# Performance work log

Measured on AMD Instinct MI355X. Metric: run time of the kernel, lower is better.

## Reference

```python
import jax, jax.numpy as jnp
import numpy as np

NBITS = 8  # num_bits_m1 == num_bits_m2 == 8


def _ste_round(x):
    # straight-through estimator round (gradient = identity)
    return x + jax.lax.stop_gradient(jnp.round(x) - x)


def _pact_quantize(x, clip_val, clip_valn, nbits):
    """PACT-style asymmetric quant-dequant with zero alignment (align_zero=True).

    clamp to [clip_valn, clip_val], affine-quantize to [0, 2^n - 1] with a
    rounded zero point, then dequantize.
    """
    levels = jnp.asarray(2 ** nbits - 1, dtype=x.dtype)
    scale = levels / (clip_val - clip_valn)
    zero_point = _ste_round(-clip_valn * scale)  # align zero to an integer level
    xc = jnp.clip(x, clip_valn, clip_val)
    q = _ste_round(xc * scale + zero_point)
    return (q - zero_point) / scale


def setup_inputs() -> dict:
    key = jax.random.key(0)
    k1, k2 = jax.random.split(key)
    B, H, S, D = 2, 16, 1024, 128
    m1 = jax.random.normal(k1, (B, H, S, D), dtype=jnp.float32)
    m2 = jax.random.normal(k2, (B, H, D, S), dtype=jnp.float32)
    return {
        "m1": m1,
        "m2": m2,
        "m1_clip_val": jnp.asarray(1.0, dtype=jnp.float32),
        "m1_clip_valn": jnp.asarray(-1.0, dtype=jnp.float32),
        "m2_clip_val": jnp.asarray(1.0, dtype=jnp.float32),
        "m2_clip_valn": jnp.asarray(-1.0, dtype=jnp.float32),
    }


def reference(m1, m2, m1_clip_val, m1_clip_valn, m2_clip_val, m2_clip_valn):
    qm1 = _pact_quantize(m1, m1_clip_val, m1_clip_valn, NBITS)
    qm2 = _pact_quantize(m2, m2_clip_val, m2_clip_valn, NBITS)
    # replaceBmm=True path: torch.matmul on [B,H,S,D] x [B,H,D,S]
    return jnp.einsum("bhsd,bhdt->bhst", qm1, qm2)
```

## Files before the change

kernel.cpp:

```cpp
#include <hip/hip_runtime.h>

typedef __attribute__((ext_vector_type(8))) short short8;
typedef __attribute__((ext_vector_type(4))) float floatx4;

__device__ __forceinline__ unsigned short quant_bf16(float x, float cvn, float cv,
                                                     float scale, float zp) {
    float xc = fminf(fmaxf(x, cvn), cv);
    float q  = rintf(xc * scale + zp);
    float v  = q - zp;
    return (unsigned short)(__float_as_uint(v) >> 16);
}

__global__ __launch_bounds__(256) void quant_m1_kernel(
        const float* __restrict__ x, unsigned short* __restrict__ q,
        const float* __restrict__ cvp, const float* __restrict__ cvnp, int n4) {
    int i = blockIdx.x * 256 + threadIdx.x;
    if (i >= n4) return;
    float cv = cvp[0], cvn = cvnp[0];
    float scale = 255.0f / (cv - cvn);
    float zp = rintf(-cvn * scale);
    floatx4 v = ((const floatx4*)x)[i];
    ushort4 o;
    o.x = quant_bf16(v[0], cvn, cv, scale, zp);
    o.y = quant_bf16(v[1], cvn, cv, scale, zp);
    o.z = quant_bf16(v[2], cvn, cv, scale, zp);
    o.w = quant_bf16(v[3], cvn, cv, scale, zp);
    ((ushort4*)q)[i] = o;
}

__global__ __launch_bounds__(256) void quant_m2t_kernel(
        const float* __restrict__ x, unsigned short* __restrict__ qt,
        const float* __restrict__ cvp, const float* __restrict__ cvnp) {
    __shared__ unsigned short ldsT[64][136];
    int batch = blockIdx.y;
    int s0 = blockIdx.x * 64;
    const float* xb = x + (size_t)batch * (128 * 1024);
    unsigned short* qb = qt + (size_t)batch * (1024 * 128);
    float cv = cvp[0], cvn = cvnp[0];
    float scale = 255.0f / (cv - cvn);
    float zp = rintf(-cvn * scale);
    int t = threadIdx.x;
#pragma unroll
    for (int r = 0; r < 2; ++r) {
        int u = t + 256 * r;
        int su = u & 15;
        int du = u >> 4;
        floatx4 v[4];
#pragma unroll
        for (int i = 0; i < 4; ++i)
            v[i] = *(const floatx4*)(xb + (size_t)(du * 4 + i) * 1024 + s0 + su * 4);
#pragma unroll
        for (int j = 0; j < 4; ++j) {
            ushort4 w;
            w.x = quant_bf16(v[0][j], cvn, cv, scale, zp);
            w.y = quant_bf16(v[1][j], cvn, cv, scale, zp);
            w.z = quant_bf16(v[2][j], cvn, cv, scale, zp);
            w.w = quant_bf16(v[3][j], cvn, cv, scale, zp);
            *(ushort4*)&ldsT[su * 4 + j][du * 4] = w;
        }
    }
    __syncthreads();
#pragma unroll
    for (int r = 0; r < 4; ++r) {
        int c = t + 256 * r;
        int sl = c >> 4, k8 = c & 15;
        *(short8*)(qb + (size_t)(s0 + sl) * 128 + k8 * 8) =
            *(const short8*)&ldsT[sl][k8 * 8];
    }
}

__global__ __launch_bounds__(256) void qbmm_kernel(
        const unsigned short* __restrict__ qA, const unsigned short* __restrict__ qBt,
        float* __restrict__ C,
        const float* __restrict__ cv1p, const float* __restrict__ cvn1p,
        const float* __restrict__ cv2p, const float* __restrict__ cvn2p) {
    int batch = blockIdx.z;
    const unsigned short* A  = qA  + (size_t)batch * (1024 * 128);
    const unsigned short* Bt = qBt + (size_t)batch * (1024 * 128);
    float* Cb = C + (size_t)batch * (1024 * 1024);
    int m0 = blockIdx.y * 128, n0 = blockIdx.x * 128;
    int tid = threadIdx.x;
    int lane = tid & 63, w = tid >> 6;
    int wr = w >> 1, wc = w & 1;
    int row16 = lane & 15, quad = lane >> 4;
    int wm = m0 + wr * 64, wn = n0 + wc * 64;

    floatx4 acc[4][4] = {};

    const short8* Ap[4];
    const short8* Bp[4];
#pragma unroll
    for (int i = 0; i < 4; ++i) {
        Ap[i] = (const short8*)(A  + (size_t)(wm + i * 16 + row16) * 128 + quad * 8);
        Bp[i] = (const short8*)(Bt + (size_t)(wn + i * 16 + row16) * 128 + quad * 8);
    }

#pragma unroll
    for (int kk = 0; kk < 4; ++kk) {
        short8 a[4], b[4];
#pragma unroll
        for (int i = 0; i < 4; ++i) { a[i] = Ap[i][kk * 4]; b[i] = Bp[i][kk * 4]; }
#pragma unroll
        for (int mi = 0; mi < 4; ++mi)
#pragma unroll
            for (int ni = 0; ni < 4; ++ni)
                acc[mi][ni] = __builtin_amdgcn_mfma_f32_16x16x32_bf16(
                    b[ni], a[mi], acc[mi][ni], 0, 0, 0);
    }

    float inv = (cv1p[0] - cvn1p[0]) * (cv2p[0] - cvn2p[0]) * (1.0f / 65025.0f);

#pragma unroll
    for (int mi = 0; mi < 4; ++mi) {
        int s = wm + mi * 16 + row16;
        float* crow = Cb + (size_t)s * 1024;
#pragma unroll
        for (int ni = 0; ni < 4; ++ni) {
            floatx4 o = acc[mi][ni] * inv;
            *(floatx4*)(crow + wn + ni * 16 + quad * 4) = o;
        }
    }
}

extern "C" void kernel_launch(void* const* d_in, const int* in_sizes, int n_in,
                              void* d_out, int out_size, void* d_ws, size_t ws_size,
                              hipStream_t stream) {
    const float* m1   = (const float*)d_in[0];
    const float* m2   = (const float*)d_in[1];
    const float* cv1  = (const float*)d_in[2];
    const float* cvn1 = (const float*)d_in[3];
    const float* cv2  = (const float*)d_in[4];
    const float* cvn2 = (const float*)d_in[5];
    float* out = (float*)d_out;

    unsigned short* qA  = (unsigned short*)d_ws;
    unsigned short* qBt = qA + 4194304;

    quant_m1_kernel<<<4096, 256, 0, stream>>>(m1, qA, cv1, cvn1, 1048576);
    quant_m2t_kernel<<<dim3(16, 32), 256, 0, stream>>>(m2, qBt, cv2, cvn2);
    qbmm_kernel<<<dim3(8, 8, 32), 256, 0, stream>>>(qA, qBt, out,
                                                    cv1, cvn1, cv2, cvn2);
}
```

Measured before the change: 191.9 us.

## Fuse quantization of both operands into the batched matmul kernel via LDS

Replaces the two quantization kernels and the separate GEMM with one kernel that loads fp32 tiles of m1 and m2, quantizes them to bf16, stages them (m2 transposed) in shared memory, then runs the MFMA loop from LDS. This removes the workspace write/read round trip and two kernel launches. In exchange each input tile is re-read and re-quantized by every block that uses it, and the larger LDS footprint may reduce occupancy.

```diff
diff --git a/kernel.cpp b/kernel.cpp
--- a/kernel.cpp
+++ b/kernel.cpp
@@ -2,6 +2,8 @@
 
 typedef __attribute__((ext_vector_type(8))) short short8;
 typedef __attribute__((ext_vector_type(4))) float floatx4;
+
+#define LDS_STRIDE 136
 
 __device__ __forceinline__ unsigned short quant_bf16(float x, float cvn, float cv,
                                                      float scale, float zp) {
@@ -11,95 +13,81 @@
     return (unsigned short)(__float_as_uint(v) >> 16);
 }
 
-__global__ __launch_bounds__(256) void quant_m1_kernel(
-        const float* __restrict__ x, unsigned short* __restrict__ q,
-        const float* __restrict__ cvp, const float* __restrict__ cvnp, int n4) {
-    int i = blockIdx.x * 256 + threadIdx.x;
-    if (i >= n4) return;
-    float cv = cvp[0], cvn = cvnp[0];
-    float scale = 255.0f / (cv - cvn);
-    float zp = rintf(-cvn * scale);
-    floatx4 v = ((const floatx4*)x)[i];
-    ushort4 o;
-    o.x = quant_bf16(v[0], cvn, cv, scale, zp);
-    o.y = quant_bf16(v[1], cvn, cv, scale, zp);
-    o.z = quant_bf16(v[2], cvn, cv, scale, zp);
-    o.w = quant_bf16(v[3], cvn, cv, scale, zp);
-    ((ushort4*)q)[i] = o;
-}
+__global__ __launch_bounds__(256) void fused_qbmm_kernel(
+        const float* __restrict__ m1, const float* __restrict__ m2,
+        float* __restrict__ C,
+        const float* __restrict__ cv1p, const float* __restrict__ cvn1p,
+        const float* __restrict__ cv2p, const float* __restrict__ cvn2p) {
+    __shared__ __align__(16) unsigned short As[128 * LDS_STRIDE];
+    __shared__ __align__(16) unsigned short Bs[128 * LDS_STRIDE];
 
-__global__ __launch_bounds__(256) void quant_m2t_kernel(
-        const float* __restrict__ x, unsigned short* __restrict__ qt,
-        const float* __restrict__ cvp, const float* __restrict__ cvnp) {
-    __shared__ unsigned short ldsT[64][136];
-    int batch = blockIdx.y;
-    int s0 = blockIdx.x * 64;
-    const float* xb = x + (size_t)batch * (128 * 1024);
-    unsigned short* qb = qt + (size_t)batch * (1024 * 128);
-    float cv = cvp[0], cvn = cvnp[0];
-    float scale = 255.0f / (cv - cvn);
-    float zp = rintf(-cvn * scale);
-    int t = threadIdx.x;
+    const int batch = blockIdx.z;
+    const int m0 = blockIdx.y * 128, n0 = blockIdx.x * 128;
+    const float* Am = m1 + (size_t)batch * (1024 * 128) + (size_t)m0 * 128;
+    const float* Bm = m2 + (size_t)batch * (128 * 1024) + n0;
+    float* Cb = C + (size_t)batch * (1024 * 1024);
+
+    const float cv1 = cv1p[0], cvn1 = cvn1p[0];
+    const float cv2 = cv2p[0], cvn2 = cvn2p[0];
+    const float s1 = 255.0f / (cv1 - cvn1);
+    const float zp1 = rintf(-cvn1 * s1);
+    const float s2 = 255.0f / (cv2 - cvn2);
+    const float zp2 = rintf(-cvn2 * s2);
+
+    const int tid = threadIdx.x;
+
+    {
+        const int col4 = tid & 31, r0 = tid >> 5;
 #pragma unroll
-    for (int r = 0; r < 2; ++r) {
-        int u = t + 256 * r;
-        int su = u & 15;
-        int du = u >> 4;
-        floatx4 v[4];
+        for (int r = 0; r < 16; ++r) {
+            const int s = r * 8 + r0;
+            floatx4 v = *(const floatx4*)(Am + (size_t)s * 128 + col4 * 4);
+            ushort4 o;
+            o.x = quant_bf16(v[0], cvn1, cv1, s1, zp1);
+            o.y = quant_bf16(v[1], cvn1, cv1, s1, zp1);
+            o.z = quant_bf16(v[2], cvn1, cv1, s1, zp1);
+            o.w = quant_bf16(v[3], cvn1, cv1, s1, zp1);
+            *(ushort4*)&As[s * LDS_STRIDE + col4 * 4] = o;
+        }
+    }
+    {
+        const int t4 = tid & 31, d0 = tid >> 5;
 #pragma unroll
-        for (int i = 0; i < 4; ++i)
-            v[i] = *(const floatx4*)(xb + (size_t)(du * 4 + i) * 1024 + s0 + su * 4);
+        for (int r = 0; r < 4; ++r) {
+            const int d4 = r * 8 + d0;
+            floatx4 v[4];
 #pragma unroll
-        for (int j = 0; j < 4; ++j) {
-            ushort4 w;
-            w.x = quant_bf16(v[0][j], cvn, cv, scale, zp);
-            w.y = quant_bf16(v[1][j], cvn, cv, scale, zp);
-            w.z = quant_bf16(v[2][j], cvn, cv, scale, zp);
-            w.w = quant_bf16(v[3][j], cvn, cv, scale, zp);
-            *(ushort4*)&ldsT[su * 4 + j][du * 4] = w;
+            for (int i = 0; i < 4; ++i)
+                v[i] = *(const floatx4*)(Bm + (size_t)(d4 * 4 + i) * 1024 + t4 * 4);
+#pragma unroll
+            for (int j = 0; j < 4; ++j) {
+                ushort4 w;
+                w.x = quant_bf16(v[0][j], cvn2, cv2, s2, zp2);
+                w.y = quant_bf16(v[1][j], cvn2, cv2, s2, zp2);
+                w.z = quant_bf16(v[2][j], cvn2, cv2, s2, zp2);
+                w.w = quant_bf16(v[3][j], cvn2, cv2, s2, zp2);
+                *(ushort4*)&Bs[(t4 * 4 + j) * LDS_STRIDE + d4 * 4] = w;
+            }
         }
     }
     __syncthreads();
-#pragma unroll
-    for (int r = 0; r < 4; ++r) {
-        int c = t + 256 * r;
-        int sl = c >> 4, k8 = c & 15;
-        *(short8*)(qb + (size_t)(s0 + sl) * 128 + k8 * 8) =
-            *(const short8*)&ldsT[sl][k8 * 8];
-    }
-}
 
-__global__ __launch_bounds__(256) void qbmm_kernel(
-        const unsigned short* __restrict__ qA, const unsigned short* __restrict__ qBt,
-        float* __restrict__ C,
-        const float* __restrict__ cv1p, const float* __restrict__ cvn1p,
-        const float* __restrict__ cv2p, const float* __restrict__ cvn2p) {
-    int batch = blockIdx.z;
-    const unsigned short* A  = qA  + (size_t)batch * (1024 * 128);
-    const unsigned short* Bt = qBt + (size_t)batch * (1024 * 128);
-    float* Cb = C + (size_t)batch * (1024 * 1024);
-    int m0 = blockIdx.y * 128, n0 = blockIdx.x * 128;
-    int tid = threadIdx.x;
-    int lane = tid & 63, w = tid >> 6;
-    int wr = w >> 1, wc = w & 1;
-    int row16 = lane & 15, quad = lane >> 4;
-    int wm = m0 + wr * 64, wn = n0 + wc * 64;
+    const int lane = tid & 63, w = tid >> 6;
+    const int wr = w >> 1, wc = w & 1;
+    const int row16 = lane & 15, quad = lane >> 4;
 
     floatx4 acc[4][4] = {};
-
-    const short8* Ap[4];
-    const short8* Bp[4];
-#pragma unroll
-    for (int i = 0; i < 4; ++i) {
-        Ap[i] = (const short8*)(A  + (size_t)(wm + i * 16 + row16) * 128 + quad * 8);
-        Bp[i] = (const short8*)(Bt + (size_t)(wn + i * 16 + row16) * 128 + quad * 8);
-    }
+    const unsigned short* Abase = &As[(wr * 64 + row16) * LDS_STRIDE + quad * 8];
+    const unsigned short* Bbase = &Bs[(wc * 64 + row16) * LDS_STRIDE + quad * 8];
 
 #pragma unroll
     for (int kk = 0; kk < 4; ++kk) {
         short8 a[4], b[4];
 #pragma unroll
-        for (int i = 0; i < 4; ++i) { a[i] = Ap[i][kk * 4]; b[i] = Bp[i][kk * 4]; }
+        for (int i = 0; i < 4; ++i) {
+            a[i] = *(const short8*)(Abase + i * 16 * LDS_STRIDE + kk * 32);
+            b[i] = *(const short8*)(Bbase + i * 16 * LDS_STRIDE + kk * 32);
+        }
 #pragma unroll
         for (int mi = 0; mi < 4; ++mi)
 #pragma unroll
@@ -108,16 +96,15 @@
                     b[ni], a[mi], acc[mi][ni], 0, 0, 0);
     }
 
-    float inv = (cv1p[0] - cvn1p[0]) * (cv2p[0] - cvn2p[0]) * (1.0f / 65025.0f);
+    const float inv = (cv1 - cvn1) * (cv2 - cvn2) * (1.0f / 65025.0f);
 
 #pragma unroll
     for (int mi = 0; mi < 4; ++mi) {
-        int s = wm + mi * 16 + row16;
-        float* crow = Cb + (size_t)s * 1024;
+        float* crow = Cb + (size_t)(m0 + wr * 64 + mi * 16 + row16) * 1024 + n0 + wc * 64;
 #pragma unroll
         for (int ni = 0; ni < 4; ++ni) {
             floatx4 o = acc[mi][ni] * inv;
-            *(floatx4*)(crow + wn + ni * 16 + quad * 4) = o;
+            *(floatx4*)(crow + ni * 16 + quad * 4) = o;
         }
     }
 }
@@ -133,11 +120,6 @@
     const float* cvn2 = (const float*)d_in[5];
     float* out = (float*)d_out;
 
-    unsigned short* qA  = (unsigned short*)d_ws;
-    unsigned short* qBt = qA + 4194304;
-
-    quant_m1_kernel<<<4096, 256, 0, stream>>>(m1, qA, cv1, cvn1, 1048576);
-    quant_m2t_kernel<<<dim3(16, 32), 256, 0, stream>>>(m2, qBt, cv2, cvn2);
-    qbmm_kernel<<<dim3(8, 8, 32), 256, 0, stream>>>(qA, qBt, out,
-                                                    cv1, cvn1, cv2, cvn2);
+    fused_qbmm_kernel<<<dim3(8, 8, 32), 256, 0, stream>>>(m1, m2, out,
+                                                          cv1, cvn1, cv2, cvn2);
 }
```

Result: no change. 194.2 us (+1.2%).
